# Optimization experiments

Hardware: AMD Instinct MI355X
Metric: run time of the kernel (lower is better)

The kernel has to match this reference:

```python
import jax, jax.numpy as jnp
import numpy as np

N, E, R = 30000, 300000, 3
IN, HID, OUT, HEADS = 256, 32, 64, 4
NEG_SLOPE = 0.2  # DGL GATConv default


def setup_inputs() -> dict:
    key = jax.random.key(0)
    ks = jax.random.split(key, 10)
    x = jax.random.normal(ks[0], (N, IN), jnp.float32)
    src = jax.random.randint(ks[1], (R, E), 0, N)
    dst = jax.random.randint(ks[2], (R, E), 0, N)
    s1 = (2.0 / IN) ** 0.5
    W1 = jax.random.normal(ks[3], (R, IN, HEADS * HID), jnp.float32) * s1
    attn_l1 = jax.random.normal(ks[4], (R, HEADS, HID), jnp.float32) * 0.1
    attn_r1 = jax.random.normal(ks[5], (R, HEADS, HID), jnp.float32) * 0.1
    b1 = jnp.zeros((R, HEADS * HID), jnp.float32)
    s2 = (2.0 / (HEADS * HID)) ** 0.5
    W2 = jax.random.normal(ks[6], (R, HEADS * HID, HEADS * OUT), jnp.float32) * s2
    attn_l2 = jax.random.normal(ks[7], (R, HEADS, OUT), jnp.float32) * 0.1
    attn_r2 = jax.random.normal(ks[8], (R, HEADS, OUT), jnp.float32) * 0.1
    b2 = jnp.zeros((R, HEADS * OUT), jnp.float32)
    return dict(x=x, src=src, dst=dst, W1=W1, attn_l1=attn_l1, attn_r1=attn_r1,
                b1=b1, W2=W2, attn_l2=attn_l2, attn_r2=attn_r2, b2=b2)


def _gat(x, s, d, W, al, ar, b):
    """Single-relation GATConv (DGL semantics): gather, edge softmax, scatter."""
    n = x.shape[0]
    H, D = al.shape
    z = (x @ W).reshape(n, H, D)                 # [n,H,D]
    el = (z * al[None]).sum(-1)                  # [n,H]
    er = (z * ar[None]).sum(-1)                  # [n,H]
    e = jax.nn.leaky_relu(el[s] + er[d], NEG_SLOPE)   # [E,H]
    m = jax.ops.segment_max(e, d, num_segments=n)     # stable edge softmax per dst
    w = jnp.exp(e - m[d])
    denom = jax.ops.segment_sum(w, d, num_segments=n)
    alpha = w / denom[d]                         # [E,H]
    out = jax.ops.segment_sum(alpha[:, :, None] * z[s], d, num_segments=n)  # [n,H,D]
    return out + b.reshape(1, H, D)


def reference(x, src, dst, W1, attn_l1, attn_r1, b1, W2, attn_l2, attn_r2, b2):
    gat_r = jax.vmap(_gat, in_axes=(None, 0, 0, 0, 0, 0, 0))
    # conv1: per-relation GAT summed across relations (HeteroGraphConv aggregate='sum')
    h = gat_r(x, src, dst, W1, attn_l1, attn_r1, b1).sum(0)      # [N,HEADS,HID]
    h = jax.nn.relu(h).reshape(-1, HEADS * HID)                  # [N,HEADS*HID]
    # conv2
    h2 = gat_r(h, src, dst, W2, attn_l2, attn_r2, b2).sum(0)     # [N,HEADS,OUT]
    return h2.mean(axis=1)                                       # [N,OUT]
```

## Files before the change

kernel.cpp:

```cpp
#include <hip/hip_runtime.h>
#include <math.h>

#define NNODES 30000
#define MPAD   30080
#define NEDGES 300000
#define NREL 3
#define IND 256
#define HIDD 32
#define OUTD 64
#define NHEADS 4
#define C1 (NHEADS*HIDD)
#define C2 (NHEADS*OUTD)
#define NEG_SLOPE 0.2f
#define CAP 64

typedef short bf16x8 __attribute__((ext_vector_type(8)));
typedef float f32x4  __attribute__((ext_vector_type(4)));

__device__ __forceinline__ float b2f(unsigned short u) {
    return __uint_as_float(((unsigned)u) << 16);
}
__device__ __forceinline__ unsigned short f2b(float f) {
    unsigned u = __float_as_uint(f);
    u += 0x7fffu + ((u >> 16) & 1u);
    return (unsigned short)(u >> 16);
}

template<int K, int N>
__device__ __forceinline__ void pack_w_dev(const float* __restrict__ W,
                                           unsigned short* __restrict__ P, int t) {
    const int KS = K / 32, NT = N / 16;
    int lane = t & 63;
    int fid = t >> 6;
    if (fid >= NREL * NT * KS) return;
    int ks = fid % KS;
    int nt = (fid / KS) % NT;
    int r  = fid / (KS * NT);
    int n  = nt * 16 + (lane & 15);
    int k0 = ks * 32 + (lane >> 4) * 8;
    const float* Wr = W + (size_t)r * K * N;
    unsigned short o[8];
#pragma unroll
    for (int j = 0; j < 8; j++) o[j] = f2b(Wr[(size_t)(k0 + j) * N + n]);
    unsigned short* dst = P + (size_t)fid * 512 + lane * 8;
    *(ushort4*)&dst[0] = *(ushort4*)&o[0];
    *(ushort4*)&dst[4] = *(ushort4*)&o[4];
}

#define CAST_BLOCKS (NNODES * IND / 4 / 256)
#define PACK1_BLOCKS (NREL * (C1/16) * (IND/32) / 4)
#define PACK2_BLOCKS (NREL * (C2/16) * (C1/32) / 4)
__global__ void prep_kernel(const float* __restrict__ x, unsigned short* __restrict__ Xh,
                            const float* __restrict__ W1, unsigned short* __restrict__ P1,
                            const float* __restrict__ W2, unsigned short* __restrict__ P2) {
    int b = blockIdx.x;
    if (b < CAST_BLOCKS) {
        int i = (b * 256 + threadIdx.x) * 4;
        float4 v = *(const float4*)&x[i];
        ushort4 o = { f2b(v.x), f2b(v.y), f2b(v.z), f2b(v.w) };
        *(ushort4*)&Xh[i] = o;
    } else if (b < CAST_BLOCKS + PACK1_BLOCKS) {
        pack_w_dev<IND, C1>(W1, P1, (b - CAST_BLOCKS) * 256 + threadIdx.x);
    } else {
        pack_w_dev<C1, C2>(W2, P2, (b - CAST_BLOCKS - PACK1_BLOCKS) * 256 + threadIdx.x);
    }
}

template<int K, int N>
__global__ __launch_bounds__(256) void mfma_gemm(
    const unsigned short* __restrict__ Ah, const unsigned short* __restrict__ Bp,
    const float* __restrict__ al, const float* __restrict__ ar,
    unsigned short* __restrict__ Zh, float* __restrict__ el, float* __restrict__ er)
{
    const int KS = K / 32, NT = N / 16, MT = 64, NP = N + 4;
    const int wave = threadIdx.x >> 6, lane = threadIdx.x & 63;
    const int r  = blockIdx.y;
    const int m0 = blockIdx.x * MT;
    const int fcol = lane & 15, quad = lane >> 4;

    __shared__ unsigned short zs[MT * (N + 4)];

    int m = m0 + wave * 16 + fcol;
    if (m >= NNODES) m = NNODES - 1;
    bf16x8 afrag[KS];
    const unsigned short* arow = Ah + (size_t)m * K + quad * 8;
#pragma unroll
    for (int ks = 0; ks < KS; ks++) afrag[ks] = *(const bf16x8*)(arow + ks * 32);

    f32x4 acc[NT];
#pragma unroll
    for (int nt = 0; nt < NT; nt++) { f32x4 z = {0.f,0.f,0.f,0.f}; acc[nt] = z; }

    const unsigned short* Bpr = Bp + (size_t)r * NT * KS * 512;
    for (int ks = 0; ks < KS; ks++) {
        bf16x8 b[NT];
#pragma unroll
        for (int nt = 0; nt < NT; nt++)
            b[nt] = *(const bf16x8*)(Bpr + ((size_t)nt * KS + ks) * 512 + lane * 8);
#pragma unroll
        for (int nt = 0; nt < NT; nt++)
            acc[nt] = __builtin_amdgcn_mfma_f32_16x16x32_bf16(afrag[ks], b[nt], acc[nt], 0, 0, 0);
    }

    {
        int lrow = wave * 16 + quad * 4;
#pragma unroll
        for (int nt = 0; nt < NT; nt++)
#pragma unroll
            for (int q = 0; q < 4; q++)
                zs[(lrow + q) * NP + nt * 16 + fcol] = f2b(acc[nt][q]);
    }
    __syncthreads();

    {
        uint2* zo = (uint2*)(Zh + ((size_t)r * MPAD + m0) * N);
        for (int i = threadIdx.x; i < MT * N / 4; i += 256) {
            int row = i / (N / 4), c4 = i % (N / 4);
            zo[i] = *(const uint2*)&zs[row * NP + c4 * 4];
        }
    }
    {
        const int D = N / NHEADS;
        int row = threadIdx.x >> 2, h = threadIdx.x & 3;
        int n = m0 + row;
        if (n < NNODES) {
            const float* alp = al + ((size_t)r * NHEADS + h) * D;
            const float* arp = ar + ((size_t)r * NHEADS + h) * D;
            const unsigned short* zp = zs + row * NP + h * D;
            float sl = 0.f, sr = 0.f;
#pragma unroll
            for (int d0 = 0; d0 < D; d0 += 4) {
                uint2 u = *(const uint2*)&zp[d0];
                float z0 = b2f((unsigned short)(u.x & 0xffff));
                float z1 = b2f((unsigned short)(u.x >> 16));
                float z2 = b2f((unsigned short)(u.y & 0xffff));
                float z3 = b2f((unsigned short)(u.y >> 16));
                sl = fmaf(z0, alp[d0], sl);     sr = fmaf(z0, arp[d0], sr);
                sl = fmaf(z1, alp[d0 + 1], sl); sr = fmaf(z1, arp[d0 + 1], sr);
                sl = fmaf(z2, alp[d0 + 2], sl); sr = fmaf(z2, arp[d0 + 2], sr);
                sl = fmaf(z3, alp[d0 + 3], sl); sr = fmaf(z3, arp[d0 + 3], sr);
            }
            el[((size_t)r * NNODES + n) * NHEADS + h] = sl;
            er[((size_t)r * NNODES + n) * NHEADS + h] = sr;
        }
    }
}

__global__ void bucket_fill(const int* __restrict__ src, const int* __restrict__ dst,
                            unsigned* __restrict__ cnt, int* __restrict__ buck) {
    int gid = blockIdx.x * blockDim.x + threadIdx.x;
    if (gid >= NREL * NEDGES) return;
    int r = gid / NEDGES;
    int d = dst[gid];
    int base = r * NNODES + d;
    unsigned pos = atomicAdd(&cnt[base], 1u);
    if (pos < CAP) buck[(size_t)base * CAP + pos] = src[gid];
}

__device__ __forceinline__ float wave_max(float t) {
#pragma unroll
    for (int o = 1; o < 64; o <<= 1) t = fmaxf(t, __shfl_xor(t, o, 64));
    return t;
}
__device__ __forceinline__ float wave_sum(float t) {
#pragma unroll
    for (int o = 1; o < 64; o <<= 1) t += __shfl_xor(t, o, 64);
    return t;
}

__global__ __launch_bounds__(256) void gat_gather1(
    const unsigned* __restrict__ cnt, const int* __restrict__ buck,
    const float* __restrict__ el, const float* __restrict__ er,
    const unsigned short* __restrict__ Zh, const float* __restrict__ b1,
    unsigned short* __restrict__ hbh)
{
    __shared__ float atab[4][4 * 65];
    int wave = threadIdx.x >> 6, lane = threadIdx.x & 63;
    int n = blockIdx.x * 4 + wave;
    if (n >= NNODES) return;
    const int h0 = lane >> 4;
    float accx = 0.f, accy = 0.f;
    for (int r = 0; r < NREL; r++) {
        int base = r * NNODES + n;
        int c = (int)cnt[base]; c = c < CAP ? c : CAP;
        if (c == 0) continue;
        int s_lane = (lane < c) ? buck[(size_t)base * CAP + lane] : -1;
        float lg[4];
        if (s_lane >= 0) {
            const float4 e4 = *(const float4*)&el[((size_t)r * NNODES + s_lane) * NHEADS];
            const float4 r4 = *(const float4*)&er[(size_t)base * NHEADS];
            float v;
            v = e4.x + r4.x; lg[0] = v > 0.f ? v : NEG_SLOPE * v;
            v = e4.y + r4.y; lg[1] = v > 0.f ? v : NEG_SLOPE * v;
            v = e4.z + r4.z; lg[2] = v > 0.f ? v : NEG_SLOPE * v;
            v = e4.w + r4.w; lg[3] = v > 0.f ? v : NEG_SLOPE * v;
        } else {
            lg[0] = lg[1] = lg[2] = lg[3] = -INFINITY;
        }
#pragma unroll
        for (int h = 0; h < 4; h++) {
            float m = wave_max(lg[h]);
            float w = (lane < c) ? __expf(lg[h] - m) : 0.f;
            float den = wave_sum(w);
            atab[wave][h * 65 + lane] = w / den;
        }
        const unsigned short* Zr = Zh + (size_t)r * MPAD * C1;
        const float* at = atab[wave] + h0 * 65;
        int j = 0;
        for (; j + 3 < c; j += 4) {
            int s0 = __builtin_amdgcn_readlane(s_lane, j);
            int s1 = __builtin_amdgcn_readlane(s_lane, j + 1);
            int s2 = __builtin_amdgcn_readlane(s_lane, j + 2);
            int s3 = __builtin_amdgcn_readlane(s_lane, j + 3);
            const ushort2 za = *(const ushort2*)&Zr[(size_t)s0 * C1 + 2 * lane];
            const ushort2 zb = *(const ushort2*)&Zr[(size_t)s1 * C1 + 2 * lane];
            const ushort2 zc = *(const ushort2*)&Zr[(size_t)s2 * C1 + 2 * lane];
            const ushort2 zd = *(const ushort2*)&Zr[(size_t)s3 * C1 + 2 * lane];
            float a0 = at[j], a1 = at[j + 1], a2 = at[j + 2], a3 = at[j + 3];
            accx = fmaf(a0, b2f(za.x), accx); accy = fmaf(a0, b2f(za.y), accy);
            accx = fmaf(a1, b2f(zb.x), accx); accy = fmaf(a1, b2f(zb.y), accy);
            accx = fmaf(a2, b2f(zc.x), accx); accy = fmaf(a2, b2f(zc.y), accy);
            accx = fmaf(a3, b2f(zd.x), accx); accy = fmaf(a3, b2f(zd.y), accy);
        }
        for (; j < c; j++) {
            int s = __builtin_amdgcn_readlane(s_lane, j);
            float a0 = at[j];
            const ushort2 z2 = *(const ushort2*)&Zr[(size_t)s * C1 + 2 * lane];
            accx = fmaf(a0, b2f(z2.x), accx);
            accy = fmaf(a0, b2f(z2.y), accy);
        }
    }
    int cch = 2 * lane;
    float bx = b1[cch]     + b1[C1 + cch]     + b1[2 * C1 + cch];
    float by = b1[cch + 1] + b1[C1 + cch + 1] + b1[2 * C1 + cch + 1];
    ushort2 o;
    o.x = f2b(fmaxf(accx + bx, 0.f));
    o.y = f2b(fmaxf(accy + by, 0.f));
    *(ushort2*)&hbh[(size_t)n * C1 + cch] = o;
}

__global__ __launch_bounds__(256) void gat_gather2(
    const unsigned* __restrict__ cnt, const int* __restrict__ buck,
    const float* __restrict__ el, const float* __restrict__ er,
    const unsigned short* __restrict__ Zh, const float* __restrict__ b2,
    float* __restrict__ out)
{
    __shared__ float atab[4][4 * 65];
    int wave = threadIdx.x >> 6, lane = threadIdx.x & 63;
    int n = blockIdx.x * 4 + wave;
    if (n >= NNODES) return;
    const int h0 = lane >> 4;
    float4 acc = {0.f, 0.f, 0.f, 0.f};
    for (int r = 0; r < NREL; r++) {
        int base = r * NNODES + n;
        int c = (int)cnt[base]; c = c < CAP ? c : CAP;
        if (c == 0) continue;
        int s_lane = (lane < c) ? buck[(size_t)base * CAP + lane] : -1;
        float lg[4];
        if (s_lane >= 0) {
            const float4 e4 = *(const float4*)&el[((size_t)r * NNODES + s_lane) * NHEADS];
            const float4 r4 = *(const float4*)&er[(size_t)base * NHEADS];
            float v;
            v = e4.x + r4.x; lg[0] = v > 0.f ? v : NEG_SLOPE * v;
            v = e4.y + r4.y; lg[1] = v > 0.f ? v : NEG_SLOPE * v;
            v = e4.z + r4.z; lg[2] = v > 0.f ? v : NEG_SLOPE * v;
            v = e4.w + r4.w; lg[3] = v > 0.f ? v : NEG_SLOPE * v;
        } else {
            lg[0] = lg[1] = lg[2] = lg[3] = -INFINITY;
        }
#pragma unroll
        for (int h = 0; h < 4; h++) {
            float m = wave_max(lg[h]);
            float w = (lane < c) ? __expf(lg[h] - m) : 0.f;
            float den = wave_sum(w);
            atab[wave][h * 65 + lane] = w / den;
        }
        const unsigned short* Zr = Zh + (size_t)r * MPAD * C2;
        const float* at = atab[wave] + h0 * 65;
        int j = 0;
        for (; j + 3 < c; j += 4) {
            int s0 = __builtin_amdgcn_readlane(s_lane, j);
            int s1 = __builtin_amdgcn_readlane(s_lane, j + 1);
            int s2 = __builtin_amdgcn_readlane(s_lane, j + 2);
            int s3 = __builtin_amdgcn_readlane(s_lane, j + 3);
            const ushort4 za = *(const ushort4*)&Zr[(size_t)s0 * C2 + 4 * lane];
            const ushort4 zb = *(const ushort4*)&Zr[(size_t)s1 * C2 + 4 * lane];
            const ushort4 zc = *(const ushort4*)&Zr[(size_t)s2 * C2 + 4 * lane];
            const ushort4 zd = *(const ushort4*)&Zr[(size_t)s3 * C2 + 4 * lane];
            float a0 = at[j], a1 = at[j + 1], a2 = at[j + 2], a3 = at[j + 3];
            acc.x = fmaf(a0, b2f(za.x), acc.x); acc.y = fmaf(a0, b2f(za.y), acc.y);
            acc.z = fmaf(a0, b2f(za.z), acc.z); acc.w = fmaf(a0, b2f(za.w), acc.w);
            acc.x = fmaf(a1, b2f(zb.x), acc.x); acc.y = fmaf(a1, b2f(zb.y), acc.y);
            acc.z = fmaf(a1, b2f(zb.z), acc.z); acc.w = fmaf(a1, b2f(zb.w), acc.w);
            acc.x = fmaf(a2, b2f(zc.x), acc.x); acc.y = fmaf(a2, b2f(zc.y), acc.y);
            acc.z = fmaf(a2, b2f(zc.z), acc.z); acc.w = fmaf(a2, b2f(zc.w), acc.w);
            acc.x = fmaf(a3, b2f(zd.x), acc.x); acc.y = fmaf(a3, b2f(zd.y), acc.y);
            acc.z = fmaf(a3, b2f(zd.z), acc.z); acc.w = fmaf(a3, b2f(zd.w), acc.w);
        }
        for (; j < c; j++) {
            int s = __builtin_amdgcn_readlane(s_lane, j);
            float a0 = at[j];
            const ushort4 z4 = *(const ushort4*)&Zr[(size_t)s * C2 + 4 * lane];
            acc.x = fmaf(a0, b2f(z4.x), acc.x);
            acc.y = fmaf(a0, b2f(z4.y), acc.y);
            acc.z = fmaf(a0, b2f(z4.z), acc.z);
            acc.w = fmaf(a0, b2f(z4.w), acc.w);
        }
    }
    int cch = 4 * lane;
#pragma unroll
    for (int q = 0; q < 4; q++) {
        float b = b2[cch + q] + b2[C2 + cch + q] + b2[2 * C2 + cch + q];
        (&acc.x)[q] += b;
    }
    acc.x += __shfl_xor(acc.x, 16, 64); acc.y += __shfl_xor(acc.y, 16, 64);
    acc.z += __shfl_xor(acc.z, 16, 64); acc.w += __shfl_xor(acc.w, 16, 64);
    acc.x += __shfl_xor(acc.x, 32, 64); acc.y += __shfl_xor(acc.y, 32, 64);
    acc.z += __shfl_xor(acc.z, 32, 64); acc.w += __shfl_xor(acc.w, 32, 64);
    if (lane < 16) {
        float4 o;
        o.x = 0.25f * acc.x; o.y = 0.25f * acc.y;
        o.z = 0.25f * acc.z; o.w = 0.25f * acc.w;
        *(float4*)&out[(size_t)n * OUTD + 4 * lane] = o;
    }
}

extern "C" void kernel_launch(void* const* d_in, const int* in_sizes, int n_in,
                              void* d_out, int out_size, void* d_ws, size_t ws_size,
                              hipStream_t stream) {
    (void)in_sizes; (void)n_in; (void)out_size; (void)ws_size;
    const float* x   = (const float*)d_in[0];
    const int*   src = (const int*)d_in[1];
    const int*   dst = (const int*)d_in[2];
    const float* W1  = (const float*)d_in[3];
    const float* al1 = (const float*)d_in[4];
    const float* ar1 = (const float*)d_in[5];
    const float* b1  = (const float*)d_in[6];
    const float* W2  = (const float*)d_in[7];
    const float* al2 = (const float*)d_in[8];
    const float* ar2 = (const float*)d_in[9];
    const float* b2  = (const float*)d_in[10];
    float* out = (float*)d_out;

    float* ws = (float*)d_ws;
    size_t off = 0;
    unsigned short* Zh  = (unsigned short*)(ws + off); off += (size_t)NREL * MPAD * C2 / 2;
    unsigned short* Xh  = (unsigned short*)(ws + off); off += (size_t)NNODES * IND / 2;
    unsigned short* hbh = (unsigned short*)(ws + off); off += (size_t)NNODES * C1 / 2;
    unsigned short* P1  = (unsigned short*)(ws + off); off += (size_t)NREL * (C1/16) * (IND/32) * 512 / 2;
    unsigned short* P2  = (unsigned short*)(ws + off); off += (size_t)NREL * (C2/16) * (C1/32) * 512 / 2;
    float* el  = ws + off; off += (size_t)NREL * NNODES * NHEADS;
    float* er  = ws + off; off += (size_t)NREL * NNODES * NHEADS;
    unsigned* cnt = (unsigned*)(ws + off); off += (size_t)NREL * NNODES;
    int* buck  = (int*)(ws + off); off += (size_t)NREL * NNODES * CAP;

    const int TB = 256;

    hipMemsetAsync(cnt, 0, (size_t)NREL * NNODES * sizeof(unsigned), stream);
    bucket_fill<<<(NREL * NEDGES + TB - 1) / TB, TB, 0, stream>>>(src, dst, cnt, buck);
    prep_kernel<<<CAST_BLOCKS + PACK1_BLOCKS + PACK2_BLOCKS, TB, 0, stream>>>(
        x, Xh, W1, P1, W2, P2);

    {
        dim3 grid(MPAD / 64, NREL);
        mfma_gemm<IND, C1><<<grid, 256, 0, stream>>>(Xh, P1, al1, ar1, Zh, el, er);
    }
    gat_gather1<<<(NNODES + 3) / 4, 256, 0, stream>>>(cnt, buck, el, er, Zh, b1, hbh);

    {
        dim3 grid(MPAD / 64, NREL);
        mfma_gemm<C1, C2><<<grid, 256, 0, stream>>>(hbh, P2, al2, ar2, Zh, el, er);
    }
    gat_gather2<<<(NNODES + 3) / 4, 256, 0, stream>>>(cnt, buck, el, er, Zh, b2, out);
}
```

Before: 365.0 us.

## Switch to fp16, fuse bucket fill into prep, hoist per-relation softmax loads

Several changes at once. Intermediate storage and the MFMA GEMMs move from bf16 to fp16. The bucket_fill kernel is folded into prep_kernel as extra blocks, which removes one launch. The gather kernels now issue the count, bucket and el/er loads for all three relations up front so their latencies overlap. Softmax reductions are cut to 16 lanes when the degree is 16 or less. fp16 has less exponent range than bf16, so large activations could overflow.

```diff
diff --git a/kernel.cpp b/kernel.cpp
--- a/kernel.cpp
+++ b/kernel.cpp
@@ -1,4 +1,5 @@
 #include <hip/hip_runtime.h>
+#include <hip/hip_fp16.h>
 #include <math.h>
 
 #define NNODES 30000
@@ -14,16 +15,14 @@
 #define NEG_SLOPE 0.2f
 #define CAP 64
 
-typedef short bf16x8 __attribute__((ext_vector_type(8)));
+typedef _Float16 f16x8 __attribute__((ext_vector_type(8)));
 typedef float f32x4  __attribute__((ext_vector_type(4)));
 
-__device__ __forceinline__ float b2f(unsigned short u) {
-    return __uint_as_float(((unsigned)u) << 16);
-}
-__device__ __forceinline__ unsigned short f2b(float f) {
-    unsigned u = __float_as_uint(f);
-    u += 0x7fffu + ((u >> 16) & 1u);
-    return (unsigned short)(u >> 16);
+__device__ __forceinline__ unsigned short f2h(float f) {
+    union { __half h; unsigned short u; } c; c.h = __float2half_rn(f); return c.u;
+}
+__device__ __forceinline__ __half2 u2h2(unsigned u) {
+    union { unsigned u; __half2 h; } c; c.u = u; return c.h;
 }
 
 template<int K, int N>
@@ -41,7 +40,7 @@
     const float* Wr = W + (size_t)r * K * N;
     unsigned short o[8];
 #pragma unroll
-    for (int j = 0; j < 8; j++) o[j] = f2b(Wr[(size_t)(k0 + j) * N + n]);
+    for (int j = 0; j < 8; j++) o[j] = f2h(Wr[(size_t)(k0 + j) * N + n]);
     unsigned short* dst = P + (size_t)fid * 512 + lane * 8;
     *(ushort4*)&dst[0] = *(ushort4*)&o[0];
     *(ushort4*)&dst[4] = *(ushort4*)&o[4];
@@ -50,19 +49,31 @@
 #define CAST_BLOCKS (NNODES * IND / 4 / 256)
 #define PACK1_BLOCKS (NREL * (C1/16) * (IND/32) / 4)
 #define PACK2_BLOCKS (NREL * (C2/16) * (C1/32) / 4)
+#define BUCK_BLOCKS  ((NREL * NEDGES + 255) / 256)
 __global__ void prep_kernel(const float* __restrict__ x, unsigned short* __restrict__ Xh,
                             const float* __restrict__ W1, unsigned short* __restrict__ P1,
-                            const float* __restrict__ W2, unsigned short* __restrict__ P2) {
+                            const float* __restrict__ W2, unsigned short* __restrict__ P2,
+                            const int* __restrict__ src, const int* __restrict__ dst,
+                            unsigned* __restrict__ cnt, int* __restrict__ buck) {
     int b = blockIdx.x;
     if (b < CAST_BLOCKS) {
         int i = (b * 256 + threadIdx.x) * 4;
         float4 v = *(const float4*)&x[i];
-        ushort4 o = { f2b(v.x), f2b(v.y), f2b(v.z), f2b(v.w) };
+        ushort4 o = { f2h(v.x), f2h(v.y), f2h(v.z), f2h(v.w) };
         *(ushort4*)&Xh[i] = o;
     } else if (b < CAST_BLOCKS + PACK1_BLOCKS) {
         pack_w_dev<IND, C1>(W1, P1, (b - CAST_BLOCKS) * 256 + threadIdx.x);
+    } else if (b < CAST_BLOCKS + PACK1_BLOCKS + PACK2_BLOCKS) {
+        pack_w_dev<C1, C2>(W2, P2, (b - CAST_BLOCKS - PACK1_BLOCKS) * 256 + threadIdx.x);
     } else {
-        pack_w_dev<C1, C2>(W2, P2, (b - CAST_BLOCKS - PACK1_BLOCKS) * 256 + threadIdx.x);
+        int gid = (b - CAST_BLOCKS - PACK1_BLOCKS - PACK2_BLOCKS) * 256 + threadIdx.x;
+        if (gid < NREL * NEDGES) {
+            int r = gid / NEDGES;
+            int d = dst[gid];
+            int base = r * NNODES + d;
+            unsigned pos = atomicAdd(&cnt[base], 1u);
+            if (pos < CAP) buck[(size_t)base * CAP + pos] = src[gid];
+        }
     }
 }
 
@@ -82,10 +93,10 @@
 
     int m = m0 + wave * 16 + fcol;
     if (m >= NNODES) m = NNODES - 1;
-    bf16x8 afrag[KS];
+    f16x8 afrag[KS];
     const unsigned short* arow = Ah + (size_t)m * K + quad * 8;
 #pragma unroll
-    for (int ks = 0; ks < KS; ks++) afrag[ks] = *(const bf16x8*)(arow + ks * 32);
+    for (int ks = 0; ks < KS; ks++) afrag[ks] = *(const f16x8*)(arow + ks * 32);
 
     f32x4 acc[NT];
 #pragma unroll
@@ -93,13 +104,13 @@
 
     const unsigned short* Bpr = Bp + (size_t)r * NT * KS * 512;
     for (int ks = 0; ks < KS; ks++) {
-        bf16x8 b[NT];
+        f16x8 b[NT];
 #pragma unroll
         for (int nt = 0; nt < NT; nt++)
-            b[nt] = *(const bf16x8*)(Bpr + ((size_t)nt * KS + ks) * 512 + lane * 8);
+            b[nt] = *(const f16x8*)(Bpr + ((size_t)nt * KS + ks) * 512 + lane * 8);
 #pragma unroll
         for (int nt = 0; nt < NT; nt++)
-            acc[nt] = __builtin_amdgcn_mfma_f32_16x16x32_bf16(afrag[ks], b[nt], acc[nt], 0, 0, 0);
+            acc[nt] = __builtin_amdgcn_mfma_f32_16x16x32_f16(afrag[ks], b[nt], acc[nt], 0, 0, 0);
     }
 
     {
@@ -108,7 +119,7 @@
         for (int nt = 0; nt < NT; nt++)
 #pragma unroll
             for (int q = 0; q < 4; q++)
-                zs[(lrow + q) * NP + nt * 16 + fcol] = f2b(acc[nt][q]);
+                zs[(lrow + q) * NP + nt * 16 + fcol] = f2h(acc[nt][q]);
     }
     __syncthreads();
 
@@ -131,10 +142,9 @@
 #pragma unroll
             for (int d0 = 0; d0 < D; d0 += 4) {
                 uint2 u = *(const uint2*)&zp[d0];
-                float z0 = b2f((unsigned short)(u.x & 0xffff));
-                float z1 = b2f((unsigned short)(u.x >> 16));
-                float z2 = b2f((unsigned short)(u.y & 0xffff));
-                float z3 = b2f((unsigned short)(u.y >> 16));
+                __half2 p0 = u2h2(u.x), p1 = u2h2(u.y);
+                float z0 = __low2float(p0), z1 = __high2float(p0);
+                float z2 = __low2float(p1), z3 = __high2float(p1);
                 sl = fmaf(z0, alp[d0], sl);     sr = fmaf(z0, arp[d0], sr);
                 sl = fmaf(z1, alp[d0 + 1], sl); sr = fmaf(z1, arp[d0 + 1], sr);
                 sl = fmaf(z2, alp[d0 + 2], sl); sr = fmaf(z2, arp[d0 + 2], sr);
@@ -146,25 +156,16 @@
     }
 }
 
-__global__ void bucket_fill(const int* __restrict__ src, const int* __restrict__ dst,
-                            unsigned* __restrict__ cnt, int* __restrict__ buck) {
-    int gid = blockIdx.x * blockDim.x + threadIdx.x;
-    if (gid >= NREL * NEDGES) return;
-    int r = gid / NEDGES;
-    int d = dst[gid];
-    int base = r * NNODES + d;
-    unsigned pos = atomicAdd(&cnt[base], 1u);
-    if (pos < CAP) buck[(size_t)base * CAP + pos] = src[gid];
-}
-
-__device__ __forceinline__ float wave_max(float t) {
-#pragma unroll
-    for (int o = 1; o < 64; o <<= 1) t = fmaxf(t, __shfl_xor(t, o, 64));
+__device__ __forceinline__ float red_max(float t, bool full) {
+#pragma unroll
+    for (int o = 1; o < 16; o <<= 1) t = fmaxf(t, __shfl_xor(t, o, 64));
+    if (full) { t = fmaxf(t, __shfl_xor(t, 16, 64)); t = fmaxf(t, __shfl_xor(t, 32, 64)); }
     return t;
 }
-__device__ __forceinline__ float wave_sum(float t) {
-#pragma unroll
-    for (int o = 1; o < 64; o <<= 1) t += __shfl_xor(t, o, 64);
+__device__ __forceinline__ float red_sum(float t, bool full) {
+#pragma unroll
+    for (int o = 1; o < 16; o <<= 1) t += __shfl_xor(t, o, 64);
+    if (full) { t += __shfl_xor(t, 16, 64); t += __shfl_xor(t, 32, 64); }
     return t;
 }
 
@@ -174,68 +175,83 @@
     const unsigned short* __restrict__ Zh, const float* __restrict__ b1,
     unsigned short* __restrict__ hbh)
 {
-    __shared__ float atab[4][4 * 65];
+    __shared__ float atab[4][NREL][4 * 65 + 3];
     int wave = threadIdx.x >> 6, lane = threadIdx.x & 63;
     int n = blockIdx.x * 4 + wave;
     if (n >= NNODES) return;
     const int h0 = lane >> 4;
+
+    int cA[NREL], slR[NREL];
+    float4 e4[NREL], r4[NREL];
+#pragma unroll
+    for (int r = 0; r < NREL; r++) {
+        int base = r * NNODES + n;
+        cA[r]  = (int)cnt[base];
+        slR[r] = buck[(size_t)base * CAP + lane];
+        r4[r]  = *(const float4*)&er[(size_t)base * NHEADS];
+    }
+#pragma unroll
+    for (int r = 0; r < NREL; r++) {
+        int c = cA[r] < CAP ? cA[r] : CAP; cA[r] = c;
+        int sS = (lane < c) ? slR[r] : 0;
+        e4[r] = *(const float4*)&el[((size_t)r * NNODES + sS) * NHEADS];
+    }
+#pragma unroll
+    for (int r = 0; r < NREL; r++) {
+        int c = cA[r]; if (c == 0) continue;
+        bool act = lane < c, full = c > 16;
+        float lg[4];
+        float v;
+        v = e4[r].x + r4[r].x; lg[0] = act ? (v > 0.f ? v : NEG_SLOPE * v) : -INFINITY;
+        v = e4[r].y + r4[r].y; lg[1] = act ? (v > 0.f ? v : NEG_SLOPE * v) : -INFINITY;
+        v = e4[r].z + r4[r].z; lg[2] = act ? (v > 0.f ? v : NEG_SLOPE * v) : -INFINITY;
+        v = e4[r].w + r4[r].w; lg[3] = act ? (v > 0.f ? v : NEG_SLOPE * v) : -INFINITY;
+#pragma unroll
+        for (int h = 0; h < 4; h++) {
+            float m = red_max(lg[h], full);
+            float w = act ? __expf(lg[h] - m) : 0.f;
+            float den = red_sum(w, full);
+            atab[wave][r][h * 65 + lane] = w / den;
+        }
+    }
     float accx = 0.f, accy = 0.f;
-    for (int r = 0; r < NREL; r++) {
-        int base = r * NNODES + n;
-        int c = (int)cnt[base]; c = c < CAP ? c : CAP;
-        if (c == 0) continue;
-        int s_lane = (lane < c) ? buck[(size_t)base * CAP + lane] : -1;
-        float lg[4];
-        if (s_lane >= 0) {
-            const float4 e4 = *(const float4*)&el[((size_t)r * NNODES + s_lane) * NHEADS];
-            const float4 r4 = *(const float4*)&er[(size_t)base * NHEADS];
-            float v;
-            v = e4.x + r4.x; lg[0] = v > 0.f ? v : NEG_SLOPE * v;
-            v = e4.y + r4.y; lg[1] = v > 0.f ? v : NEG_SLOPE * v;
-            v = e4.z + r4.z; lg[2] = v > 0.f ? v : NEG_SLOPE * v;
-            v = e4.w + r4.w; lg[3] = v > 0.f ? v : NEG_SLOPE * v;
-        } else {
-            lg[0] = lg[1] = lg[2] = lg[3] = -INFINITY;
-        }
-#pragma unroll
-        for (int h = 0; h < 4; h++) {
-            float m = wave_max(lg[h]);
-            float w = (lane < c) ? __expf(lg[h] - m) : 0.f;
-            float den = wave_sum(w);
-            atab[wave][h * 65 + lane] = w / den;
-        }
+#pragma unroll
+    for (int r = 0; r < NREL; r++) {
+        int c = cA[r]; if (c == 0) continue;
+        int s_lane = slR[r];
         const unsigned short* Zr = Zh + (size_t)r * MPAD * C1;
-        const float* at = atab[wave] + h0 * 65;
+        const float* at = atab[wave][r] + h0 * 65;
         int j = 0;
         for (; j + 3 < c; j += 4) {
             int s0 = __builtin_amdgcn_readlane(s_lane, j);
             int s1 = __builtin_amdgcn_readlane(s_lane, j + 1);
             int s2 = __builtin_amdgcn_readlane(s_lane, j + 2);
             int s3 = __builtin_amdgcn_readlane(s_lane, j + 3);
-            const ushort2 za = *(const ushort2*)&Zr[(size_t)s0 * C1 + 2 * lane];
-            const ushort2 zb = *(const ushort2*)&Zr[(size_t)s1 * C1 + 2 * lane];
-            const ushort2 zc = *(const ushort2*)&Zr[(size_t)s2 * C1 + 2 * lane];
-            const ushort2 zd = *(const ushort2*)&Zr[(size_t)s3 * C1 + 2 * lane];
+            unsigned ua = *(const unsigned*)&Zr[(size_t)s0 * C1 + 2 * lane];
+            unsigned ub = *(const unsigned*)&Zr[(size_t)s1 * C1 + 2 * lane];
+            unsigned uc = *(const unsigned*)&Zr[(size_t)s2 * C1 + 2 * lane];
+            unsigned ud = *(const unsigned*)&Zr[(size_t)s3 * C1 + 2 * lane];
             float a0 = at[j], a1 = at[j + 1], a2 = at[j + 2], a3 = at[j + 3];
-            accx = fmaf(a0, b2f(za.x), accx); accy = fmaf(a0, b2f(za.y), accy);
-            accx = fmaf(a1, b2f(zb.x), accx); accy = fmaf(a1, b2f(zb.y), accy);
-            accx = fmaf(a2, b2f(zc.x), accx); accy = fmaf(a2, b2f(zc.y), accy);
-            accx = fmaf(a3, b2f(zd.x), accx); accy = fmaf(a3, b2f(zd.y), accy);
+            __half2 za = u2h2(ua), zb = u2h2(ub), zc = u2h2(uc), zd = u2h2(ud);
+            accx = fmaf(a0, __low2float(za), accx); accy = fmaf(a0, __high2float(za), accy);
+            accx = fmaf(a1, __low2float(zb), accx); accy = fmaf(a1, __high2float(zb), accy);
+            accx = fmaf(a2, __low2float(zc), accx); accy = fmaf(a2, __high2float(zc), accy);
+            accx = fmaf(a3, __low2float(zd), accx); accy = fmaf(a3, __high2float(zd), accy);
         }
         for (; j < c; j++) {
             int s = __builtin_amdgcn_readlane(s_lane, j);
             float a0 = at[j];
-            const ushort2 z2 = *(const ushort2*)&Zr[(size_t)s * C1 + 2 * lane];
-            accx = fmaf(a0, b2f(z2.x), accx);
-            accy = fmaf(a0, b2f(z2.y), accy);
+            __half2 z2 = u2h2(*(const unsigned*)&Zr[(size_t)s * C1 + 2 * lane]);
+            accx = fmaf(a0, __low2float(z2), accx);
+            accy = fmaf(a0, __high2float(z2), accy);
         }
     }
     int cch = 2 * lane;
     float bx = b1[cch]     + b1[C1 + cch]     + b1[2 * C1 + cch];
     float by = b1[cch + 1] + b1[C1 + cch + 1] + b1[2 * C1 + cch + 1];
     ushort2 o;
-    o.x = f2b(fmaxf(accx + bx, 0.f));
-    o.y = f2b(fmaxf(accy + by, 0.f));
+    o.x = f2h(fmaxf(accx + bx, 0.f));
+    o.y = f2h(fmaxf(accy + by, 0.f));
     *(ushort2*)&hbh[(size_t)n * C1 + cch] = o;
 }
 
@@ -245,66 +261,82 @@
     const unsigned short* __restrict__ Zh, const float* __restrict__ b2,
     float* __restrict__ out)
 {
-    __shared__ float atab[4][4 * 65];
+    __shared__ float atab[4][NREL][4 * 65 + 3];
     int wave = threadIdx.x >> 6, lane = threadIdx.x & 63;
     int n = blockIdx.x * 4 + wave;
     if (n >= NNODES) return;
     const int h0 = lane >> 4;
+
+    int cA[NREL], slR[NREL];
+    float4 e4[NREL], r4[NREL];
+#pragma unroll
+    for (int r = 0; r < NREL; r++) {
+        int base = r * NNODES + n;
+        cA[r]  = (int)cnt[base];
+        slR[r] = buck[(size_t)base * CAP + lane];
+        r4[r]  = *(const float4*)&er[(size_t)base * NHEADS];
+    }
+#pragma unroll
+    for (int r = 0; r < NREL; r++) {
+        int c = cA[r] < CAP ? cA[r] : CAP; cA[r] = c;
+        int sS = (lane < c) ? slR[r] : 0;
+        e4[r] = *(const float4*)&el[((size_t)r * NNODES + sS) * NHEADS];
+    }
+#pragma unroll
+    for (int r = 0; r < NREL; r++) {
+        int c = cA[r]; if (c == 0) continue;
+        bool act = lane < c, full = c > 16;
+        float lg[4];
+        float v;
+        v = e4[r].x + r4[r].x; lg[0] = act ? (v > 0.f ? v : NEG_SLOPE * v) : -INFINITY;
+        v = e4[r].y + r4[r].y; lg[1] = act ? (v > 0.f ? v : NEG_SLOPE * v) : -INFINITY;
+        v = e4[r].z + r4[r].z; lg[2] = act ? (v > 0.f ? v : NEG_SLOPE * v) : -INFINITY;
+        v = e4[r].w + r4[r].w; lg[3] = act ? (v > 0.f ? v : NEG_SLOPE * v) : -INFINITY;
+#pragma unroll
+        for (int h = 0; h < 4; h++) {
+            float m = red_max(lg[h], full);
+            float w = act ? __expf(lg[h] - m) : 0.f;
+            float den = red_sum(w, full);
+            atab[wave][r][h * 65 + lane] = w / den;
+        }
+    }
     float4 acc = {0.f, 0.f, 0.f, 0.f};
-    for (int r = 0; r < NREL; r++) {
-        int base = r * NNODES + n;
-        int c = (int)cnt[base]; c = c < CAP ? c : CAP;
-        if (c == 0) continue;
-        int s_lane = (lane < c) ? buck[(size_t)base * CAP + lane] : -1;
-        float lg[4];
-        if (s_lane >= 0) {
-            const float4 e4 = *(const float4*)&el[((size_t)r * NNODES + s_lane) * NHEADS];
-            const float4 r4 = *(const float4*)&er[(size_t)base * NHEADS];
-            float v;
-            v = e4.x + r4.x; lg[0] = v > 0.f ? v : NEG_SLOPE * v;
-            v = e4.y + r4.y; lg[1] = v > 0.f ? v : NEG_SLOPE * v;
-            v = e4.z + r4.z; lg[2] = v > 0.f ? v : NEG_SLOPE * v;
-            v = e4.w + r4.w; lg[3] = v > 0.f ? v : NEG_SLOPE * v;
-        } else {
-            lg[0] = lg[1] = lg[2] = lg[3] = -INFINITY;
-        }
-#pragma unroll
-        for (int h = 0; h < 4; h++) {
-            float m = wave_max(lg[h]);
-            float w = (lane < c) ? __expf(lg[h] - m) : 0.f;
-            float den = wave_sum(w);
-            atab[wave][h * 65 + lane] = w / den;
-        }
+#pragma unroll
+    for (int r = 0; r < NREL; r++) {
+        int c = cA[r]; if (c == 0) continue;
+        int s_lane = slR[r];
         const unsigned short* Zr = Zh + (size_t)r * MPAD * C2;
-        const float* at = atab[wave] + h0 * 65;
+        const float* at = atab[wave][r] + h0 * 65;
         int j = 0;
         for (; j + 3 < c; j += 4) {
             int s0 = __builtin_amdgcn_readlane(s_lane, j);
             int s1 = __builtin_amdgcn_readlane(s_lane, j + 1);
             int s2 = __builtin_amdgcn_readlane(s_lane, j + 2);
             int s3 = __builtin_amdgcn_readlane(s_lane, j + 3);
-            const ushort4 za = *(const ushort4*)&Zr[(size_t)s0 * C2 + 4 * lane];
-            const ushort4 zb = *(const ushort4*)&Zr[(size_t)s1 * C2 + 4 * lane];
-            const ushort4 zc = *(const ushort4*)&Zr[(size_t)s2 * C2 + 4 * lane];
-            const ushort4 zd = *(const ushort4*)&Zr[(size_t)s3 * C2 + 4 * lane];
+            uint2 ua = *(const uint2*)&Zr[(size_t)s0 * C2 + 4 * lane];
+            uint2 ub = *(const uint2*)&Zr[(size_t)s1 * C2 + 4 * lane];
+            uint2 uc = *(const uint2*)&Zr[(size_t)s2 * C2 + 4 * lane];
+            uint2 ud = *(const uint2*)&Zr[(size_t)s3 * C2 + 4 * lane];
             float a0 = at[j], a1 = at[j + 1], a2 = at[j + 2], a3 = at[j + 3];
-            acc.x = fmaf(a0, b2f(za.x), acc.x); acc.y = fmaf(a0, b2f(za.y), acc.y);
-            acc.z = fmaf(a0, b2f(za.z), acc.z); acc.w = fmaf(a0, b2f(za.w), acc.w);
-            acc.x = fmaf(a1, b2f(zb.x), acc.x); acc.y = fmaf(a1, b2f(zb.y), acc.y);
-            acc.z = fmaf(a1, b2f(zb.z), acc.z); acc.w = fmaf(a1, b2f(zb.w), acc.w);
-            acc.x = fmaf(a2, b2f(zc.x), acc.x); acc.y = fmaf(a2, b2f(zc.y), acc.y);
-            acc.z = fmaf(a2, b2f(zc.z), acc.z); acc.w = fmaf(a2, b2f(zc.w), acc.w);
-            acc.x = fmaf(a3, b2f(zd.x), acc.x); acc.y = fmaf(a3, b2f(zd.y), acc.y);
-            acc.z = fmaf(a3, b2f(zd.z), acc.z); acc.w = fmaf(a3, b2f(zd.w), acc.w);
+            __half2 p;
+            p = u2h2(ua.x); acc.x = fmaf(a0, __low2float(p), acc.x); acc.y = fmaf(a0, __high2float(p), acc.y);
+            p = u2h2(ua.y); acc.z = fmaf(a0, __low2float(p), acc.z); acc.w = fmaf(a0, __high2float(p), acc.w);
+            p = u2h2(ub.x); acc.x = fmaf(a1, __low2float(p), acc.x); acc.y = fmaf(a1, __high2float(p), acc.y);
+            p = u2h2(ub.y); acc.z = fmaf(a1, __low2float(p), acc.z); acc.w = fmaf(a1, __high2float(p), acc.w);
+            p = u2h2(uc.x); acc.x = fmaf(a2, __low2float(p), acc.x); acc.y = fmaf(a2, __high2float(p), acc.y);
+            p = u2h2(uc.y); acc.z = fmaf(a2, __low2float(p), acc.z); acc.w = fmaf(a2, __high2float(p), acc.w);
+            p = u2h2(ud.x); acc.x = fmaf(a3, __low2float(p), acc.x); acc.y = fmaf(a3, __high2float(p), acc.y);
+            p = u2h2(ud.y); acc.z = fmaf(a3, __low2float(p), acc.z); acc.w = fmaf(a3, __high2float(p), acc.w);
         }
         for (; j < c; j++) {
             int s = __builtin_amdgcn_readlane(s_lane, j);
             float a0 = at[j];
-            const ushort4 z4 = *(const ushort4*)&Zr[(size_t)s * C2 + 4 * lane];
-            acc.x = fmaf(a0, b2f(z4.x), acc.x);
-            acc.y = fmaf(a0, b2f(z4.y), acc.y);
-            acc.z = fmaf(a0, b2f(z4.z), acc.z);
-            acc.w = fmaf(a0, b2f(z4.w), acc.w);
+            uint2 u = *(const uint2*)&Zr[(size_t)s * C2 + 4 * lane];
+            __half2 p0 = u2h2(u.x), p1 = u2h2(u.y);
+            acc.x = fmaf(a0, __low2float(p0), acc.x);
+            acc.y = fmaf(a0, __high2float(p0), acc.y);
+            acc.z = fmaf(a0, __low2float(p1), acc.z);
+            acc.w = fmaf(a0, __high2float(p1), acc.w);
         }
     }
     int cch = 4 * lane;
@@ -357,9 +389,8 @@
     const int TB = 256;
 
     hipMemsetAsync(cnt, 0, (size_t)NREL * NNODES * sizeof(unsigned), stream);
-    bucket_fill<<<(NREL * NEDGES + TB - 1) / TB, TB, 0, stream>>>(src, dst, cnt, buck);
-    prep_kernel<<<CAST_BLOCKS + PACK1_BLOCKS + PACK2_BLOCKS, TB, 0, stream>>>(
-        x, Xh, W1, P1, W2, P2);
+    prep_kernel<<<CAST_BLOCKS + PACK1_BLOCKS + PACK2_BLOCKS + BUCK_BLOCKS, TB, 0, stream>>>(
+        x, Xh, W1, P1, W2, P2, src, dst, cnt, buck);
 
     {
         dim3 grid(MPAD / 64, NREL);
```

Measured after the change: 374.2 us. +2.5%, slower.
